# Optimization experiments

Hardware: AMD Instinct MI355X
Metric: run time of the kernel (lower is better)

Reference implementation:

```python
import jax, jax.numpy as jnp
import numpy as np

NSQ = 3  # lstm_num_square


def setup_inputs() -> dict:
    key = jax.random.key(0)
    k1, k2, k3, k4, k5 = jax.random.split(key, 5)
    B, C, T, H = 64, 2, 128, 96
    blk = H // NSQ
    V = blk * blk  # downsample.version = 1024
    x = jax.random.normal(k1, (B, C, T, H, H), dtype=jnp.float32)
    # Per-block LSTM params, hidden_size=1, gate order (i, f, g, o) as in PyTorch.
    # PyTorch init: uniform(-1/sqrt(hidden), 1/sqrt(hidden)) = uniform(-1, 1) here.
    W_ih = jax.random.uniform(k2, (NSQ, NSQ, 4, V), minval=-1.0, maxval=1.0, dtype=jnp.float32)
    W_hh = jax.random.uniform(k3, (NSQ, NSQ, 4), minval=-1.0, maxval=1.0, dtype=jnp.float32)
    b_ih = jax.random.uniform(k4, (NSQ, NSQ, 4), minval=-1.0, maxval=1.0, dtype=jnp.float32)
    b_hh = jax.random.uniform(k5, (NSQ, NSQ, 4), minval=-1.0, maxval=1.0, dtype=jnp.float32)
    return {"x": x, "W_ih": W_ih, "W_hh": W_hh, "b_ih": b_ih, "b_hh": b_hh}


def reference(x, W_ih, W_hh, b_ih, b_hh):
    # x: (B, C, T, H, H); only channel 0 is used (as in the original module).
    B, _, T, H, _ = x.shape
    blk = H // NSQ
    V = blk * blk
    # Downsample: split HxH grid into NSQ x NSQ blocks, flatten each block.
    xs = x[:, 0].reshape(B, T, NSQ, blk, NSQ, blk)
    xs = xs.transpose(1, 0, 2, 4, 3, 5).reshape(T, B, NSQ, NSQ, V)  # (T,B,n,n,V)
    # Precompute input contributions to all 4 gates for all blocks at once.
    x_gates = jnp.einsum('tbijv,ijgv->tbijg', xs, W_ih) + b_ih + b_hh  # (T,B,n,n,4)

    def step(carry, xg):
        h, c = carry  # each (B, n, n), hidden_size = 1 per block
        g = xg + W_hh * h[..., None]  # (B,n,n,4)
        i = jax.nn.sigmoid(g[..., 0])
        f = jax.nn.sigmoid(g[..., 1])
        gg = jnp.tanh(g[..., 2])
        o = jax.nn.sigmoid(g[..., 3])
        c = f * c + i * gg
        h = o * jnp.tanh(c)
        return (h, c), h

    h0 = jnp.zeros((B, NSQ, NSQ), dtype=x.dtype)
    c0 = jnp.zeros((B, NSQ, NSQ), dtype=x.dtype)
    _, hs = jax.lax.scan(step, (h0, c0), x_gates)
    return hs  # (T, B, NSQ, NSQ)
```

## Files before the change

kernel.cpp:

```cpp
#include <hip/hip_runtime.h>

#define T_LEN 128
#define B_SZ  64
#define NC    9
#define H_SZ  96
#define V_SZ  1024
#define MT    8

__global__ __launch_bounds__(256) void gates_kernel(
    const float* __restrict__ x,
    const float* __restrict__ W_ih,
    float* __restrict__ xg)
{
    const int lane  = threadIdx.x & 63;
    const int wid   = threadIdx.x >> 6;
    const int wave  = blockIdx.x * 4 + wid;
    const int cell  = wave >> 10;
    const int chunk = wave & 1023;
    const int i = cell / 3, j = cell % 3;

    float4 wf[4][4];
    const float* wbase = W_ih + (size_t)cell * 4 * V_SZ;
    #pragma unroll
    for (int k = 0; k < 4; ++k) {
        const int v = k * 256 + lane * 4;
        #pragma unroll
        for (int g = 0; g < 4; ++g)
            wf[k][g] = *(const float4*)(wbase + g * V_SZ + v);
    }

    const int p0 = lane >> 3;
    const int q0 = (lane & 7) * 4;
    const int rowcol = (i * 32) * H_SZ + j * 32 + q0;

    const int tb0 = chunk * MT;

    float4 xv[4];
    {
        const int t = tb0 >> 6, b = tb0 & 63;
        const float* slab = x + ((size_t)(b * 2) * T_LEN + t) * (H_SZ * H_SZ) + rowcol;
        #pragma unroll
        for (int k = 0; k < 4; ++k)
            xv[k] = *(const float4*)(slab + (k * 8 + p0) * H_SZ);
    }

    #pragma unroll
    for (int m = 0; m < MT; ++m) {
        float4 nx[4];
        if (m + 1 < MT) {
            const int tbn = tb0 + m + 1;
            const int t = tbn >> 6, b = tbn & 63;
            const float* slab = x + ((size_t)(b * 2) * T_LEN + t) * (H_SZ * H_SZ) + rowcol;
            #pragma unroll
            for (int k = 0; k < 4; ++k)
                nx[k] = *(const float4*)(slab + (k * 8 + p0) * H_SZ);
        }

        float a0 = 0.f, a1 = 0.f, a2 = 0.f, a3 = 0.f;
        #pragma unroll
        for (int k = 0; k < 4; ++k) {
            const float4 v = xv[k];
            a0 = fmaf(v.x, wf[k][0].x, fmaf(v.y, wf[k][0].y, fmaf(v.z, wf[k][0].z, fmaf(v.w, wf[k][0].w, a0))));
            a1 = fmaf(v.x, wf[k][1].x, fmaf(v.y, wf[k][1].y, fmaf(v.z, wf[k][1].z, fmaf(v.w, wf[k][1].w, a1))));
            a2 = fmaf(v.x, wf[k][2].x, fmaf(v.y, wf[k][2].y, fmaf(v.z, wf[k][2].z, fmaf(v.w, wf[k][2].w, a2))));
            a3 = fmaf(v.x, wf[k][3].x, fmaf(v.y, wf[k][3].y, fmaf(v.z, wf[k][3].z, fmaf(v.w, wf[k][3].w, a3))));
        }

        const bool m1 = (lane & 1) != 0;
        float y01 = m1 ? a0 : a1;
        float a01 = (m1 ? a1 : a0) + __shfl_xor(y01, 1, 64);
        float y23 = m1 ? a2 : a3;
        float a23 = (m1 ? a3 : a2) + __shfl_xor(y23, 1, 64);
        const bool m2 = (lane & 2) != 0;
        float ys = m2 ? a01 : a23;
        float s  = (m2 ? a23 : a01) + __shfl_xor(ys, 2, 64);
        s += __shfl_xor(s, 4, 64);
        s += __shfl_xor(s, 8, 64);
        s += __shfl_xor(s, 16, 64);
        s += __shfl_xor(s, 32, 64);

        if (lane < 4)
            xg[((size_t)(tb0 + m) * NC + cell) * 4 + lane] = s;

        #pragma unroll
        for (int k = 0; k < 4; ++k) xv[k] = nx[k];
    }
}

__device__ __forceinline__ float fsig(float xx) {
    return __builtin_amdgcn_rcpf(1.f + __expf(-xx));
}
__device__ __forceinline__ float ftanh(float xx) {
    return fmaf(-2.f, __builtin_amdgcn_rcpf(1.f + __expf(2.f * xx)), 1.f);
}

__global__ __launch_bounds__(64) void scan_kernel(
    const float* __restrict__ xg,
    const float* __restrict__ W_hh,
    const float* __restrict__ b_ih,
    const float* __restrict__ b_hh,
    float* __restrict__ out)
{
    const int tid  = blockIdx.x * 64 + threadIdx.x;
    const int cell = tid % 9;

    const float4 wh = *(const float4*)(W_hh + cell * 4);
    const float4 bi = *(const float4*)(b_ih + cell * 4);
    const float4 bh = *(const float4*)(b_hh + cell * 4);
    const float bx = bi.x + bh.x, by = bi.y + bh.y, bz = bi.z + bh.z, bw = bi.w + bh.w;

    const float4* xg4 = (const float4*)xg;

    float h = 0.f, c = 0.f;
    float4 g = xg4[tid];
    for (int t = 0; t < T_LEN; ++t) {
        const int tn = (t + 1 < T_LEN) ? t + 1 : t;
        const float4 gn = xg4[(size_t)tn * (B_SZ * NC) + tid];

        const float gi = fmaf(wh.x, h, g.x + bx);
        const float gf = fmaf(wh.y, h, g.y + by);
        const float gz = fmaf(wh.z, h, g.z + bz);
        const float go = fmaf(wh.w, h, g.w + bw);

        const float ii = fsig(gi);
        const float ff = fsig(gf);
        const float gt = ftanh(gz);
        const float oo = fsig(go);

        c = fmaf(ff, c, ii * gt);
        h = oo * ftanh(c);

        out[(size_t)t * (B_SZ * NC) + tid] = h;
        g = gn;
    }
}

extern "C" void kernel_launch(void* const* d_in, const int* in_sizes, int n_in,
                              void* d_out, int out_size, void* d_ws, size_t ws_size,
                              hipStream_t stream) {
    const float* x    = (const float*)d_in[0];
    const float* W_ih = (const float*)d_in[1];
    const float* W_hh = (const float*)d_in[2];
    const float* b_ih = (const float*)d_in[3];
    const float* b_hh = (const float*)d_in[4];
    float* out = (float*)d_out;

    float* xg = (float*)d_ws;

    gates_kernel<<<dim3((NC * (T_LEN * B_SZ / MT)) / 4), dim3(256), 0, stream>>>(x, W_ih, xg);
    scan_kernel<<<dim3(NC), dim3(64), 0, stream>>>(xg, W_hh, b_ih, b_hh, out);
}
```

Before: 734.6 us.

## Fuse gate projection and LSTM scan into one per-batch-cell kernel

New measurement: 722.7 us. Within noise of the previous version (-1.6%).

```diff
diff --git a/kernel.cpp b/kernel.cpp
--- a/kernel.cpp
+++ b/kernel.cpp
@@ -1,22 +1,32 @@
 #include <hip/hip_runtime.h>
+
 
 #define T_LEN 128
 #define B_SZ  64
 #define NC    9
 #define H_SZ  96
 #define V_SZ  1024
-#define MT    8
+#define SLAB  (H_SZ * H_SZ)
 
-__global__ __launch_bounds__(256) void gates_kernel(
+__device__ __forceinline__ float fsig(float xx) {
+    return __builtin_amdgcn_rcpf(1.f + __expf(-xx));
+}
+__device__ __forceinline__ float ftanh(float xx) {
+    return fmaf(-2.f, __builtin_amdgcn_rcpf(1.f + __expf(2.f * xx)), 1.f);
+}
+
+__global__ __launch_bounds__(64) void fused_lstm_kernel(
     const float* __restrict__ x,
     const float* __restrict__ W_ih,
-    float* __restrict__ xg)
+    const float* __restrict__ W_hh,
+    const float* __restrict__ b_ih,
+    const float* __restrict__ b_hh,
+    float* __restrict__ out)
 {
-    const int lane  = threadIdx.x & 63;
-    const int wid   = threadIdx.x >> 6;
-    const int wave  = blockIdx.x * 4 + wid;
-    const int cell  = wave >> 10;
-    const int chunk = wave & 1023;
+    const int lane = threadIdx.x;
+    const int bc   = blockIdx.x;
+    const int cell = bc % 9;
+    const int b    = bc / 9;
     const int i = cell / 3, j = cell % 3;
 
     float4 wf[4][4];
@@ -28,34 +38,31 @@
         for (int g = 0; g < 4; ++g)
             wf[k][g] = *(const float4*)(wbase + g * V_SZ + v);
     }
+    const float4 wh = *(const float4*)(W_hh + cell * 4);
+    const float4 bi = *(const float4*)(b_ih + cell * 4);
+    const float4 bh = *(const float4*)(b_hh + cell * 4);
+    const float bx = bi.x + bh.x, by2 = bi.y + bh.y;
+    const float bz = bi.z + bh.z, bw  = bi.w + bh.w;
 
     const int p0 = lane >> 3;
     const int q0 = (lane & 7) * 4;
-    const int rowcol = (i * 32) * H_SZ + j * 32 + q0;
+    const float* slab0 = x + (size_t)(b * 2) * T_LEN * SLAB
+                           + (i * 32) * H_SZ + j * 32 + q0;
 
-    const int tb0 = chunk * MT;
+    const bool pb0 = (lane & 1) != 0;
+    const bool pb1 = (lane & 2) != 0;
 
-    float4 xv[4];
-    {
-        const int t = tb0 >> 6, b = tb0 & 63;
-        const float* slab = x + ((size_t)(b * 2) * T_LEN + t) * (H_SZ * H_SZ) + rowcol;
+    float h = 0.f, c = 0.f;
+    float4 P0[4], P1[4], P2[4], P3[4];
+
+    auto LOADT = [&](float4 (&buf)[4], int tt) {
+        const float* sp = slab0 + (size_t)tt * SLAB;
         #pragma unroll
         for (int k = 0; k < 4; ++k)
-            xv[k] = *(const float4*)(slab + (k * 8 + p0) * H_SZ);
-    }
+            buf[k] = *(const float4*)(sp + (k * 8 + p0) * H_SZ);
+    };
 
-    #pragma unroll
-    for (int m = 0; m < MT; ++m) {
-        float4 nx[4];
-        if (m + 1 < MT) {
-            const int tbn = tb0 + m + 1;
-            const int t = tbn >> 6, b = tbn & 63;
-            const float* slab = x + ((size_t)(b * 2) * T_LEN + t) * (H_SZ * H_SZ) + rowcol;
-            #pragma unroll
-            for (int k = 0; k < 4; ++k)
-                nx[k] = *(const float4*)(slab + (k * 8 + p0) * H_SZ);
-        }
-
+    auto STEPT = [&](const float4 (&xv)[4], int t) {
         float a0 = 0.f, a1 = 0.f, a2 = 0.f, a3 = 0.f;
         #pragma unroll
         for (int k = 0; k < 4; ++k) {
@@ -65,73 +72,48 @@
             a2 = fmaf(v.x, wf[k][2].x, fmaf(v.y, wf[k][2].y, fmaf(v.z, wf[k][2].z, fmaf(v.w, wf[k][2].w, a2))));
             a3 = fmaf(v.x, wf[k][3].x, fmaf(v.y, wf[k][3].y, fmaf(v.z, wf[k][3].z, fmaf(v.w, wf[k][3].w, a3))));
         }
-
-        const bool m1 = (lane & 1) != 0;
-        float y01 = m1 ? a0 : a1;
-        float a01 = (m1 ? a1 : a0) + __shfl_xor(y01, 1, 64);
-        float y23 = m1 ? a2 : a3;
-        float a23 = (m1 ? a3 : a2) + __shfl_xor(y23, 1, 64);
-        const bool m2 = (lane & 2) != 0;
-        float ys = m2 ? a01 : a23;
-        float s  = (m2 ? a23 : a01) + __shfl_xor(ys, 2, 64);
+        float y01 = pb0 ? a0 : a1;
+        float a01 = (pb0 ? a1 : a0) + __shfl_xor(y01, 1, 64);
+        float y23 = pb0 ? a2 : a3;
+        float a23 = (pb0 ? a3 : a2) + __shfl_xor(y23, 1, 64);
+        float ys = pb1 ? a01 : a23;
+        float s  = (pb1 ? a23 : a01) + __shfl_xor(ys, 2, 64);
         s += __shfl_xor(s, 4, 64);
         s += __shfl_xor(s, 8, 64);
         s += __shfl_xor(s, 16, 64);
         s += __shfl_xor(s, 32, 64);
+        const float y1 = __shfl_xor(s, 1, 64);
+        const float y2 = __shfl_xor(s, 2, 64);
+        const float y3 = __shfl_xor(y1, 2, 64);
+        const float G0 = pb1 ? (pb0 ? y3 : y2) : (pb0 ? y1 : s);
+        const float G1 = pb1 ? (pb0 ? y2 : y3) : (pb0 ? s : y1);
+        const float G2 = pb1 ? (pb0 ? y1 : s) : (pb0 ? y3 : y2);
+        const float G3 = pb1 ? (pb0 ? s : y1) : (pb0 ? y2 : y3);
 
-        if (lane < 4)
-            xg[((size_t)(tb0 + m) * NC + cell) * 4 + lane] = s;
-
-        #pragma unroll
-        for (int k = 0; k < 4; ++k) xv[k] = nx[k];
-    }
-}
-
-__device__ __forceinline__ float fsig(float xx) {
-    return __builtin_amdgcn_rcpf(1.f + __expf(-xx));
-}
-__device__ __forceinline__ float ftanh(float xx) {
-    return fmaf(-2.f, __builtin_amdgcn_rcpf(1.f + __expf(2.f * xx)), 1.f);
-}
-
-__global__ __launch_bounds__(64) void scan_kernel(
-    const float* __restrict__ xg,
-    const float* __restrict__ W_hh,
-    const float* __restrict__ b_ih,
-    const float* __restrict__ b_hh,
-    float* __restrict__ out)
-{
-    const int tid  = blockIdx.x * 64 + threadIdx.x;
-    const int cell = tid % 9;
-
-    const float4 wh = *(const float4*)(W_hh + cell * 4);
-    const float4 bi = *(const float4*)(b_ih + cell * 4);
-    const float4 bh = *(const float4*)(b_hh + cell * 4);
-    const float bx = bi.x + bh.x, by = bi.y + bh.y, bz = bi.z + bh.z, bw = bi.w + bh.w;
-
-    const float4* xg4 = (const float4*)xg;
-
-    float h = 0.f, c = 0.f;
-    float4 g = xg4[tid];
-    for (int t = 0; t < T_LEN; ++t) {
-        const int tn = (t + 1 < T_LEN) ? t + 1 : t;
-        const float4 gn = xg4[(size_t)tn * (B_SZ * NC) + tid];
-
-        const float gi = fmaf(wh.x, h, g.x + bx);
-        const float gf = fmaf(wh.y, h, g.y + by);
-        const float gz = fmaf(wh.z, h, g.z + bz);
-        const float go = fmaf(wh.w, h, g.w + bw);
-
+        const float gi = fmaf(wh.x, h, G0 + bx);
+        const float gf = fmaf(wh.y, h, G1 + by2);
+        const float gz = fmaf(wh.z, h, G2 + bz);
+        const float go = fmaf(wh.w, h, G3 + bw);
         const float ii = fsig(gi);
         const float ff = fsig(gf);
         const float gt = ftanh(gz);
         const float oo = fsig(go);
-
         c = fmaf(ff, c, ii * gt);
         h = oo * ftanh(c);
+        if (lane == 0) out[(size_t)t * (B_SZ * NC) + bc] = h;
+    };
 
-        out[(size_t)t * (B_SZ * NC) + tid] = h;
-        g = gn;
+    LOADT(P0, 0);
+    LOADT(P1, 1);
+    for (int t = 0; t < T_LEN; t += 4) {
+        if (t + 2 < T_LEN) LOADT(P2, t + 2);
+        STEPT(P0, t);
+        if (t + 3 < T_LEN) LOADT(P3, t + 3);
+        STEPT(P1, t + 1);
+        if (t + 4 < T_LEN) LOADT(P0, t + 4);
+        STEPT(P2, t + 2);
+        if (t + 5 < T_LEN) LOADT(P1, t + 5);
+        STEPT(P3, t + 3);
     }
 }
 
@@ -145,8 +127,8 @@
     const float* b_hh = (const float*)d_in[4];
     float* out = (float*)d_out;
 
-    float* xg = (float*)d_ws;
+    (void)d_ws; (void)ws_size;
 
-    gates_kernel<<<dim3((NC * (T_LEN * B_SZ / MT)) / 4), dim3(256), 0, stream>>>(x, W_ih, xg);
-    scan_kernel<<<dim3(NC), dim3(64), 0, stream>>>(xg, W_hh, b_ih, b_hh, out);
+    fused_lstm_kernel<<<dim3(B_SZ * NC), dim3(64), 0, stream>>>(
+        x, W_ih, W_hh, b_ih, b_hh, out);
 }
```
